# Performance work log

Measured on AMD Instinct MI355X. Metric: run time of the kernel, lower is better.

Reference implementation:

```python
import jax, jax.numpy as jnp
import numpy as np

IMG = 14          # image_x_y_dim
STRIDE = 4        # stride == kernel_size == n_qubits
H_MAT = jnp.array([[1.0, 1.0], [1.0, -1.0]], dtype=jnp.complex64) / np.sqrt(2.0)
_RZ_SIGNS = jnp.array([-0.5j, 0.5j], dtype=jnp.complex64)


def _apply_1q(state, U, w):
    # contract 2x2 gate U into wire-axis w of state with shape (2,)*n
    s = jnp.tensordot(U, state, axes=[[1], [w]])
    return jnp.moveaxis(s, 0, w)


def _rz(state, theta, w, n):
    d = jnp.exp(_RZ_SIGNS * theta)  # diag(e^{-i t/2}, e^{i t/2})
    shape = [1] * n
    shape[w] = 2
    return state * d.reshape(shape)


def _rx(state, theta, w):
    c = jnp.cos(0.5 * theta).astype(jnp.complex64)
    s = ((-1j) * jnp.sin(0.5 * theta)).astype(jnp.complex64)
    U = jnp.stack([jnp.stack([c, s]), jnp.stack([s, c])])
    return _apply_1q(state, U, w)


def _ry(state, theta, w):
    c = jnp.cos(0.5 * theta).astype(jnp.complex64)
    s = jnp.sin(0.5 * theta).astype(jnp.complex64)
    U = jnp.stack([jnp.stack([c, -s]), jnp.stack([s, c])])
    return _apply_1q(state, U, w)


def _crz(state, theta, cw, tw, n):
    # PennyLane CRZ: diag(1, 1, e^{-i t/2}, e^{i t/2}) in |control, target> basis
    d = jnp.exp(_RZ_SIGNS * theta)
    P = jnp.stack([jnp.ones(2, jnp.complex64), d])  # axes: (control, target)
    if cw > tw:
        P = P.T
    a, b = min(cw, tw), max(cw, tw)
    shape = [1] * n
    shape[a] = 2
    shape[b] = 2
    return state * P.reshape(shape)


def _zexp(state, n):
    probs = state.real ** 2 + state.imag ** 2
    outs = []
    for w in range(n):
        shape = [1] * n
        shape[w] = 2
        sgn = jnp.array([1.0, -1.0], jnp.float32).reshape(shape)
        outs.append(jnp.sum(probs * sgn))
    return jnp.stack(outs)  # (n,)


def _circuit4(x, weights):
    # x: (L,) with L in {4, 8, 16}; weights: (2, 8)
    n, vpq, L = 4, 4, x.shape[0]
    state = jnp.zeros((2,) * n, jnp.complex64).at[(0,) * n].set(1.0)
    for q in range(n):  # encoding: H then alternating RZ/RX per qubit
        state = _apply_1q(state, H_MAT, q)
        for i in range(vpq):
            idx = q * vpq + i
            if idx < L:
                state = _rz(state, x[idx], q, n) if i % 2 == 0 else _rx(state, x[idx], q)
    for l in range(2):  # n_layers
        for i in range(n):
            state = _crz(state, weights[l, i], i, (i + 1) % n, n)
        for j in range(n, 2 * n):
            state = _ry(state, weights[l, j], j % n)
    return _zexp(state, n)  # (4,)


def _circuit8(x, weights):
    # x: (64,); weights: (3, 16); angles scaled by pi as in qnn_circuit
    n, L = 8, 64
    vpq = L // n + 1  # 9
    state = jnp.zeros((2,) * n, jnp.complex64).at[(0,) * n].set(1.0)
    for q in range(n):
        state = _apply_1q(state, H_MAT, q)
        for i in range(vpq):
            idx = q * vpq + i
            if idx < L:
                theta = np.pi * x[idx]
                state = _rz(state, theta, q, n) if i % 2 == 0 else _rx(state, theta, q)
    for l in range(3):  # qnn_layers
        for i in range(n):
            state = _crz(state, weights[l, i], i, (i + 1) % n, n)
        for j in range(n, 2 * n):
            state = _ry(state, weights[l, j], j % n)
    return _zexp(state, n)  # (8,)


def _forward_single(x196, w1, w2, fc_w, fc_b):
    img = x196.reshape(IMG, IMG)
    feats = []
    for i in range(0, IMG, STRIDE):
        for j in range(0, IMG, STRIDE):
            patch = img[i:i + 4, j:j + 4].reshape(-1)  # edge patches truncate to 8 or 4
            feats.append(_circuit4(patch, w1))
    f = jnp.concatenate(feats)       # (64,)
    g = _circuit8(f, w2)             # (8,)
    return fc_w @ g + fc_b           # (3,)


def setup_inputs() -> dict:
    key = jax.random.key(0)
    k0, k1, k2, k3, k4 = jax.random.split(key, 5)
    bs = 8192
    X = jax.random.normal(k0, (bs, 196), jnp.float32)
    w1 = jax.random.uniform(k1, (2, 8), jnp.float32, 0.0, 2.0 * np.pi)
    w2 = jax.random.uniform(k2, (3, 16), jnp.float32, 0.0, 2.0 * np.pi)
    fc_w = jax.random.normal(k3, (3, 8), jnp.float32) / np.sqrt(8.0)
    fc_b = jax.random.normal(k4, (3,), jnp.float32) * 0.01
    return {"X": X, "w1": w1, "w2": w2, "fc_w": fc_w, "fc_b": fc_b}


def reference(X, w1, w2, fc_w, fc_b):
    return jax.vmap(_forward_single, in_axes=(0, None, None, None, None))(X, w1, w2, fc_w, fc_b)
```

## Files before the change

### kernel.cpp

```cpp
#include <hip/hip_runtime.h>

#define DEV __device__ __forceinline__

namespace {

typedef float f32x2 __attribute__((ext_vector_type(2)));

DEV f32x2 splat(float x){ f32x2 r; r.x = x; r.y = x; return r; }
DEV f32x2 csw(f32x2 a){ return __builtin_shufflevector(a, a, 1, 0); }
DEV f32x2 cmulv(f32x2 a, f32x2 b){
  f32x2 nt; nt.x = -b.y; nt.y = b.x;
  return splat(a.x)*b + splat(a.y)*nt;
}
DEV f32x2 cconj(f32x2 a){ a.y = -a.y; return a; }
DEV f32x2 cphase(f32x2 a, f32x2 cv, f32x2 sv){ return cv*a + sv*csw(a); }
DEV void halfsc(float th, float& c, float& s){ __sincosf(0.5f*th, &s, &c); }

constexpr float RSQRT2 = 0.70710678118654752440f;
constexpr float PI_F   = 3.14159265358979323846f;

template<int CTRL> DEV float qperm(float v){
  return __int_as_float(__builtin_amdgcn_mov_dpp(__float_as_int(v), CTRL, 0xF, 0xF, true));
}
template<int OFF> DEV float swzf(float v){
  return __int_as_float(__builtin_amdgcn_ds_swizzle(__float_as_int(v), OFF));
}
template<int B> DEV float shfx(float v){
  if constexpr (B==1)      return qperm<0xB1>(v);
  else if constexpr (B==2) return qperm<0x4E>(v);
  else if constexpr (B==4) return swzf<0x101F>(v);
  else if constexpr (B==8) return qperm<0x128>(v);
  else                     return swzf<0x401F>(v);
}

template<int I0, int N> DEV void run_gates(f32x2 (&v)[2], const float* f, float scale){
  #pragma unroll
  for (int i = I0; i < I0 + N; ++i){
    float c, s; halfsc(scale * f[i], c, s);
    f32x2 cv = splat(c);
    f32x2 sp; sp.x = s;  sp.y = -s;
    if ((i & 1) == 0){
      f32x2 sn; sn.x = -s; sn.y = s;
      v[0] = cv*v[0] + sp*csw(v[0]);
      v[1] = cv*v[1] + sn*csw(v[1]);
    } else {
      f32x2 t0 = csw(v[0]), t1 = csw(v[1]);
      v[0] = cv*v[0] + sp*t1;
      v[1] = cv*v[1] + sp*t0;
    }
  }
}
template<int N> DEV void build_psi(f32x2 (&v)[2], const float* ang, float scale){
  v[0].x = RSQRT2; v[0].y = 0.f;
  v[1].x = RSQRT2; v[1].y = 0.f;
  run_gates<0, N>(v, ang, scale);
}

template<int S> DEV void ry_loc8(f32x2 (&a)[8], float2 cs){
  const float c = cs.x, s = cs.y;
  #pragma unroll
  for (int m = 0; m < 8; ++m) if (!(m & S)) {
    f32x2 u = a[m], v = a[m|S];
    a[m]   = splat(c)*u - splat(s)*v;
    a[m|S] = splat(s)*u + splat(c)*v;
  }
}
template<int MASK> DEV void ry_lane8(f32x2 (&a)[8], int r, float2 cs){
  const float c = cs.x;
  const float sg = (r & MASK) ? cs.y : -cs.y;
  #pragma unroll
  for (int m = 0; m < 8; ++m){
    f32x2 o; o.x = shfx<MASK>(a[m].x); o.y = shfx<MASK>(a[m].y);
    a[m] = splat(c)*a[m] + splat(sg)*o;
  }
}

DEV f32x2 tov(float2 v){ f32x2 r; r.x = v.x; r.y = v.y; return r; }

}

__global__ __launch_bounds__(256, 5)
void qnn_fused_kernel(const float* __restrict__ X,  const float* __restrict__ w1,
                      const float* __restrict__ w2, const float* __restrict__ fcw,
                      const float* __restrict__ fcb, float* __restrict__ out, int bs)
{
  __shared__ float  feats[8][80];
  __shared__ float4 p1chain[8][16][5];
  __shared__ float4 chainH[8][8][2];
  __shared__ float4 chain2[8][9];
  __shared__ float4 p1phi[2][2][8];
  __shared__ float2 p1ry[2][4];
  __shared__ float2 ryw[3][8];
  __shared__ float4 phi2[3*32*9];

  const int t  = threadIdx.x;
  const int sl = t >> 5;
  const int r  = t & 31;
  int sample = blockIdx.x * 8 + sl;
  if (sample >= bs) sample = bs - 1;

  if (t < 32){
    const int l = t >> 4, Lb = (t >> 3) & 1, m = t & 7;
    const float h0 = 0.5f*w1[l*8+0], h1 = 0.5f*w1[l*8+1];
    const float h2 = 0.5f*w1[l*8+2], h3 = 0.5f*w1[l*8+3];
    const bool m4 = m & 4, m2 = m & 2, m1 = m & 1;
    float phi = 0.f;
    phi += Lb ? (m4 ? h0 : -h0) : 0.f;
    phi += m4 ? (m2 ? h1 : -h1) : 0.f;
    phi += m2 ? (m1 ? h2 : -h2) : 0.f;
    phi += m1 ? (Lb ? h3 : -h3) : 0.f;
    float c, s; __sincosf(phi, &s, &c);
    p1phi[l][Lb][m] = {c, c, -s, s};
  } else if (t < 40){
    const int j = t - 32, l = j >> 2, i = j & 3;
    float c, s; halfsc(w1[l*8 + 4 + i], c, s); p1ry[l][i] = {c, s};
  } else if (t < 64){
    const int j = t - 40, l = j >> 3, i = j & 7;
    float c, s; halfsc(w2[l*16 + 8 + i], c, s); ryw[l][i] = {c, s};
  }
  for (int idx = t; idx < 3*256; idx += 256){
    const int l = idx >> 8, rr = (idx >> 3) & 31, mm = idx & 7;
    const float* wl = w2 + l*16;
    const float h0 = 0.5f*wl[0], h1 = 0.5f*wl[1], h2 = 0.5f*wl[2], h3 = 0.5f*wl[3];
    const float h4 = 0.5f*wl[4], h5 = 0.5f*wl[5], h6 = 0.5f*wl[6], h7 = 0.5f*wl[7];
    const bool b16 = rr & 16, b8 = rr & 8, b4 = rr & 4, b2 = rr & 2, b1 = rr & 1;
    const bool m4 = mm & 4, m2 = mm & 2, m1 = mm & 1;
    float phi = 0.f;
    phi += b16 ? (b8 ? h0 : -h0) : 0.f;
    phi += b8  ? (b4 ? h1 : -h1) : 0.f;
    phi += b4  ? (b2 ? h2 : -h2) : 0.f;
    phi += b2  ? (b1 ? h3 : -h3) : 0.f;
    phi += b1  ? (m4 ? h4 : -h4) : 0.f;
    phi += m4  ? (m2 ? h5 : -h5) : 0.f;
    phi += m2  ? (m1 ? h6 : -h6) : 0.f;
    phi += m1  ? (b16 ? h7 : -h7) : 0.f;
    float c, s; __sincosf(phi, &s, &c);
    phi2[(l*32 + rr)*9 + mm] = {c, c, -s, s};
  }

  #pragma unroll
  for (int jj = 0; jj < 2; ++jj){
    const int j = t + jj*256;
    const int s_ = j >> 6, p = (j >> 2) & 15, q = j & 3;
    const int pi = p >> 2, pj = p & 3;
    const int shift = (pj == 3) ? 1 : 2;
    const int cmask = (1 << shift) - 1;
    const int limit = ((pi == 3) ? 2 : 4) << shift;
    int gs = blockIdx.x * 8 + s_;
    if (gs >= bs) gs = bs - 1;
    const float* Xf = X + (size_t)gs * 196;
    float ang[4];
    #pragma unroll
    for (int i = 0; i < 4; ++i){
      const int k = q*4 + i;
      int idx = (pi*4 + (k >> shift))*14 + pj*4 + (k & cmask);
      idx = idx > 195 ? 195 : idx;
      float v = Xf[idx];
      ang[i] = (k < limit) ? v : 0.f;
    }
    f32x2 v[2];
    build_psi<4>(v, ang, 1.0f);
    p1chain[s_][p][q] = {v[0].x, v[0].y, v[1].x, v[1].y};
  }
  __syncthreads();

  {
    const int p = r >> 1, Lb = r & 1;
    f32x2 ps[4][2];
    #pragma unroll
    for (int q = 0; q < 4; ++q){
      float4 fq = p1chain[sl][p][q];
      ps[q][0].x = fq.x; ps[q][0].y = fq.y;
      ps[q][1].x = fq.z; ps[q][1].y = fq.w;
    }
    f32x2 a8[8];
    {
      f32x2 t12[4];
      #pragma unroll
      for (int j = 0; j < 4; ++j) t12[j] = cmulv(ps[1][j>>1], ps[2][j&1]);
      f32x2 base = Lb ? ps[0][1] : ps[0][0];
      f32x2 bt[4];
      #pragma unroll
      for (int j = 0; j < 4; ++j) bt[j] = cmulv(base, t12[j]);
      #pragma unroll
      for (int m = 0; m < 8; ++m) a8[m] = cmulv(bt[m>>1], ps[3][m&1]);
    }

    #pragma unroll
    for (int l = 0; l < 2; ++l){
      const float4* ph = &p1phi[l][Lb][0];
      #pragma unroll
      for (int m = 0; m < 8; ++m){
        float4 w = ph[m];
        f32x2 cv; cv.x = w.x; cv.y = w.y;
        f32x2 sv; sv.x = w.z; sv.y = w.w;
        a8[m] = cphase(a8[m], cv, sv);
      }
      ry_lane8<1>(a8, r, p1ry[l][0]);
      ry_loc8<4>(a8, p1ry[l][1]);
      ry_loc8<2>(a8, p1ry[l][2]);
      ry_loc8<1>(a8, p1ry[l][3]);
    }

    float pr8[8];
    #pragma unroll
    for (int m = 0; m < 8; ++m) pr8[m] = a8[m].x*a8[m].x + a8[m].y*a8[m].y;
    float s_loc = 0.f;
    #pragma unroll
    for (int m = 0; m < 8; ++m) s_loc += pr8[m];
    float e1 = 0.f, e2 = 0.f, e3 = 0.f;
    #pragma unroll
    for (int m = 0; m < 8; ++m){
      e1 += (m & 4) ? -pr8[m] : pr8[m];
      e2 += (m & 2) ? -pr8[m] : pr8[m];
      e3 += (m & 1) ? -pr8[m] : pr8[m];
    }
    float v0 = Lb ? -s_loc : s_loc;
    v0 += shfx<1>(v0); e1 += shfx<1>(e1); e2 += shfx<1>(e2); e3 += shfx<1>(e3);
    feats[sl][p*4 + 2*Lb + 0] = Lb ? e2 : v0;
    feats[sl][p*4 + 2*Lb + 1] = Lb ? e3 : e1;
    if (r < 16) feats[sl][64 + r] = 0.f;
  }
  __syncthreads();

  if (t < 128){
    const int h = t >> 6, jj = t & 63;
    const int s_ = jj >> 3, c = jj & 7;
    const float* f = &feats[s_][c*9];
    f32x2 v[2];
    if (h == 0){
      build_psi<5>(v, f, PI_F);
    } else {
      v[0].x = 1.f; v[0].y = 0.f;
      v[1].x = 0.f; v[1].y = 0.f;
      run_gates<5, 4>(v, f, PI_F);
    }
    chainH[s_][c][h] = {v[0].x, v[0].y, v[1].x, v[1].y};
  }
  __syncthreads();
  if (t < 64){
    const int s_ = t >> 3, c = t & 7;
    float4 A = chainH[s_][c][0], B = chainH[s_][c][1];
    f32x2 vA0, vA1, al, be;
    vA0.x=A.x; vA0.y=A.y; vA1.x=A.z; vA1.y=A.w;
    al.x=B.x;  al.y=B.y;  be.x=B.z;  be.y=B.w;
    f32x2 v0 = cmulv(al, vA0) - cmulv(cconj(be), vA1);
    f32x2 v1 = cmulv(be, vA0) + cmulv(cconj(al), vA1);
    chain2[s_][c] = {v0.x, v0.y, v1.x, v1.y};
  }
  __syncthreads();

  f32x2 a[8];
  {
    const float2* c2 = (const float2*)&chain2[sl][0];
    f32x2 e0 = tov(c2[0*2 + ((r>>4)&1)]);
    f32x2 e1 = tov(c2[1*2 + ((r>>3)&1)]);
    f32x2 e2 = tov(c2[2*2 + ((r>>2)&1)]);
    f32x2 e3 = tov(c2[3*2 + ((r>>1)&1)]);
    f32x2 e4 = tov(c2[4*2 + ( r    &1)]);
    f32x2 L  = cmulv(cmulv(cmulv(e0, e1), cmulv(e2, e3)), e4);

    float4 q5 = chain2[sl][5], q6 = chain2[sl][6], q7 = chain2[sl][7];
    f32x2 p5[2], p6[2], p7[2];
    p5[0].x=q5.x; p5[0].y=q5.y; p5[1].x=q5.z; p5[1].y=q5.w;
    p6[0].x=q6.x; p6[0].y=q6.y; p6[1].x=q6.z; p6[1].y=q6.w;
    p7[0].x=q7.x; p7[0].y=q7.y; p7[1].x=q7.z; p7[1].y=q7.w;
    f32x2 p56[4];
    #pragma unroll
    for (int j = 0; j < 4; ++j) p56[j] = cmulv(p5[j>>1], p6[j&1]);
    f32x2 Lp[4];
    #pragma unroll
    for (int j = 0; j < 4; ++j) Lp[j] = cmulv(L, p56[j]);
    #pragma unroll
    for (int m = 0; m < 8; ++m) a[m] = cmulv(Lp[m>>1], p7[m&1]);
  }

  #pragma unroll
  for (int l = 0; l < 3; ++l){
    const float4* ph = &phi2[(l*32 + r)*9];
    #pragma unroll
    for (int m = 0; m < 8; ++m){
      float4 w = ph[m];
      f32x2 cv; cv.x = w.x; cv.y = w.y;
      f32x2 sv; sv.x = w.z; sv.y = w.w;
      a[m] = cphase(a[m], cv, sv);
    }
    ry_lane8<16>(a, r, ryw[l][0]);
    ry_lane8<8>(a, r, ryw[l][1]);
    ry_lane8<4>(a, r, ryw[l][2]);
    ry_lane8<2>(a, r, ryw[l][3]);
    ry_lane8<1>(a, r, ryw[l][4]);
    ry_loc8<4>(a, ryw[l][5]);
    ry_loc8<2>(a, ryw[l][6]);
    ry_loc8<1>(a, ryw[l][7]);
  }

  float pr8[8];
  #pragma unroll
  for (int m = 0; m < 8; ++m) pr8[m] = a[m].x*a[m].x + a[m].y*a[m].y;
  float s_loc = 0.f;
  #pragma unroll
  for (int m = 0; m < 8; ++m) s_loc += pr8[m];
  float e5 = 0.f, e6 = 0.f, e7 = 0.f;
  #pragma unroll
  for (int m = 0; m < 8; ++m){
    e5 += (m & 4) ? -pr8[m] : pr8[m];
    e6 += (m & 2) ? -pr8[m] : pr8[m];
    e7 += (m & 1) ? -pr8[m] : pr8[m];
  }
  float gp[8];
  gp[0] = (r & 16) ? -s_loc : s_loc;
  gp[1] = (r &  8) ? -s_loc : s_loc;
  gp[2] = (r &  4) ? -s_loc : s_loc;
  gp[3] = (r &  2) ? -s_loc : s_loc;
  gp[4] = (r &  1) ? -s_loc : s_loc;
  gp[5] = e5; gp[6] = e6; gp[7] = e7;

  float o0 = 0.f, o1 = 0.f, o2 = 0.f;
  #pragma unroll
  for (int w = 0; w < 8; ++w){
    o0 += fcw[0*8 + w] * gp[w];
    o1 += fcw[1*8 + w] * gp[w];
    o2 += fcw[2*8 + w] * gp[w];
  }
  o0 += shfx<1>(o0);  o1 += shfx<1>(o1);  o2 += shfx<1>(o2);
  o0 += shfx<2>(o0);  o1 += shfx<2>(o1);  o2 += shfx<2>(o2);
  o0 += shfx<4>(o0);  o1 += shfx<4>(o1);  o2 += shfx<4>(o2);
  o0 += shfx<8>(o0);  o1 += shfx<8>(o1);  o2 += shfx<8>(o2);
  o0 += shfx<16>(o0); o1 += shfx<16>(o1); o2 += shfx<16>(o2);

  if (r < 3){
    float o = (r == 0) ? o0 : ((r == 1) ? o1 : o2);
    out[(size_t)sample*3 + r] = o + fcb[r];
  }
}

extern "C" void kernel_launch(void* const* d_in, const int* in_sizes, int n_in,
                              void* d_out, int out_size, void* d_ws, size_t ws_size,
                              hipStream_t stream)
{
  const float* X   = (const float*)d_in[0];
  const float* w1  = (const float*)d_in[1];
  const float* w2  = (const float*)d_in[2];
  const float* fcw = (const float*)d_in[3];
  const float* fcb = (const float*)d_in[4];
  float* out = (float*)d_out;
  const int bs = in_sizes[0] / 196;
  const int blocks = (bs + 7) / 8;
  hipLaunchKernelGGL(qnn_fused_kernel, dim3(blocks), dim3(256), 0, stream,
                     X, w1, w2, fcw, fcb, out, bs);
}
```

Measured before the change: 17.99 us.

## Process 16 samples per block with 16 amplitudes per lane

```diff
diff --git a/kernel.cpp b/kernel.cpp
--- a/kernel.cpp
+++ b/kernel.cpp
@@ -13,7 +13,10 @@
   return splat(a.x)*b + splat(a.y)*nt;
 }
 DEV f32x2 cconj(f32x2 a){ a.y = -a.y; return a; }
-DEV f32x2 cphase(f32x2 a, f32x2 cv, f32x2 sv){ return cv*a + sv*csw(a); }
+DEV f32x2 cphase2(f32x2 a, float c, float s){
+  f32x2 sv; sv.x = -s; sv.y = s;
+  return splat(c)*a + sv*csw(a);
+}
 DEV void halfsc(float th, float& c, float& s){ __sincosf(0.5f*th, &s, &c); }
 
 constexpr float RSQRT2 = 0.70710678118654752440f;
@@ -29,8 +32,7 @@
   if constexpr (B==1)      return qperm<0xB1>(v);
   else if constexpr (B==2) return qperm<0x4E>(v);
   else if constexpr (B==4) return swzf<0x101F>(v);
-  else if constexpr (B==8) return qperm<0x128>(v);
-  else                     return swzf<0x401F>(v);
+  else                     return qperm<0x128>(v);
 }
 
 template<int I0, int N> DEV void run_gates(f32x2 (&v)[2], const float* f, float scale){
@@ -56,20 +58,20 @@
   run_gates<0, N>(v, ang, scale);
 }
 
-template<int S> DEV void ry_loc8(f32x2 (&a)[8], float2 cs){
+template<int S> DEV void ry_loc16(f32x2 (&a)[16], float2 cs){
   const float c = cs.x, s = cs.y;
   #pragma unroll
-  for (int m = 0; m < 8; ++m) if (!(m & S)) {
+  for (int m = 0; m < 16; ++m) if (!(m & S)) {
     f32x2 u = a[m], v = a[m|S];
     a[m]   = splat(c)*u - splat(s)*v;
     a[m|S] = splat(s)*u + splat(c)*v;
   }
 }
-template<int MASK> DEV void ry_lane8(f32x2 (&a)[8], int r, float2 cs){
+template<int MASK> DEV void ry_lane16(f32x2 (&a)[16], int r, float2 cs){
   const float c = cs.x;
   const float sg = (r & MASK) ? cs.y : -cs.y;
   #pragma unroll
-  for (int m = 0; m < 8; ++m){
+  for (int m = 0; m < 16; ++m){
     f32x2 o; o.x = shfx<MASK>(a[m].x); o.y = shfx<MASK>(a[m].y);
     a[m] = splat(c)*a[m] + splat(sg)*o;
   }
@@ -79,38 +81,38 @@
 
 }
 
-__global__ __launch_bounds__(256, 5)
+__global__ __launch_bounds__(256, 2)
 void qnn_fused_kernel(const float* __restrict__ X,  const float* __restrict__ w1,
                       const float* __restrict__ w2, const float* __restrict__ fcw,
                       const float* __restrict__ fcb, float* __restrict__ out, int bs)
 {
-  __shared__ float  feats[8][80];
-  __shared__ float4 p1chain[8][16][5];
-  __shared__ float4 chainH[8][8][2];
-  __shared__ float4 chain2[8][9];
-  __shared__ float4 p1phi[2][2][8];
+  __shared__ float  feats[16][80];
+  __shared__ float4 p1chain[16][16][5];
+  __shared__ float4 chainH[16][8][2];
+  __shared__ float4 chain2[16][9];
+  __shared__ float2 p1phi2[2][16];
   __shared__ float2 p1ry[2][4];
   __shared__ float2 ryw[3][8];
-  __shared__ float4 phi2[3*32*9];
+  __shared__ float2 phi2[3*16*18];
 
   const int t  = threadIdx.x;
-  const int sl = t >> 5;
-  const int r  = t & 31;
-  int sample = blockIdx.x * 8 + sl;
+  const int sl = t >> 4;
+  const int r  = t & 15;
+  int sample = blockIdx.x * 16 + sl;
   if (sample >= bs) sample = bs - 1;
 
   if (t < 32){
-    const int l = t >> 4, Lb = (t >> 3) & 1, m = t & 7;
+    const int l = t >> 4, m = t & 15;
     const float h0 = 0.5f*w1[l*8+0], h1 = 0.5f*w1[l*8+1];
     const float h2 = 0.5f*w1[l*8+2], h3 = 0.5f*w1[l*8+3];
-    const bool m4 = m & 4, m2 = m & 2, m1 = m & 1;
+    const bool b0 = m & 8, b1 = m & 4, b2 = m & 2, b3 = m & 1;
     float phi = 0.f;
-    phi += Lb ? (m4 ? h0 : -h0) : 0.f;
-    phi += m4 ? (m2 ? h1 : -h1) : 0.f;
-    phi += m2 ? (m1 ? h2 : -h2) : 0.f;
-    phi += m1 ? (Lb ? h3 : -h3) : 0.f;
+    phi += b0 ? (b1 ? h0 : -h0) : 0.f;
+    phi += b1 ? (b2 ? h1 : -h1) : 0.f;
+    phi += b2 ? (b3 ? h2 : -h2) : 0.f;
+    phi += b3 ? (b0 ? h3 : -h3) : 0.f;
     float c, s; __sincosf(phi, &s, &c);
-    p1phi[l][Lb][m] = {c, c, -s, s};
+    p1phi2[l][m] = {c, s};
   } else if (t < 40){
     const int j = t - 32, l = j >> 2, i = j & 3;
     float c, s; halfsc(w1[l*8 + 4 + i], c, s); p1ry[l][i] = {c, s};
@@ -118,35 +120,34 @@
     const int j = t - 40, l = j >> 3, i = j & 7;
     float c, s; halfsc(w2[l*16 + 8 + i], c, s); ryw[l][i] = {c, s};
   }
-  for (int idx = t; idx < 3*256; idx += 256){
-    const int l = idx >> 8, rr = (idx >> 3) & 31, mm = idx & 7;
+  #pragma unroll
+  for (int jj = 0; jj < 3; ++jj){
+    const int idx = t + jj*256;
+    const int l = idx >> 8, rr = (idx >> 4) & 15, mm = idx & 15;
     const float* wl = w2 + l*16;
-    const float h0 = 0.5f*wl[0], h1 = 0.5f*wl[1], h2 = 0.5f*wl[2], h3 = 0.5f*wl[3];
-    const float h4 = 0.5f*wl[4], h5 = 0.5f*wl[5], h6 = 0.5f*wl[6], h7 = 0.5f*wl[7];
-    const bool b16 = rr & 16, b8 = rr & 8, b4 = rr & 4, b2 = rr & 2, b1 = rr & 1;
-    const bool m4 = mm & 4, m2 = mm & 2, m1 = mm & 1;
+    float h[8];
+    #pragma unroll
+    for (int i = 0; i < 8; ++i) h[i] = 0.5f*wl[i];
+    bool b[8];
+    b[0]=(rr>>3)&1; b[1]=(rr>>2)&1; b[2]=(rr>>1)&1; b[3]=rr&1;
+    b[4]=(mm>>3)&1; b[5]=(mm>>2)&1; b[6]=(mm>>1)&1; b[7]=mm&1;
     float phi = 0.f;
-    phi += b16 ? (b8 ? h0 : -h0) : 0.f;
-    phi += b8  ? (b4 ? h1 : -h1) : 0.f;
-    phi += b4  ? (b2 ? h2 : -h2) : 0.f;
-    phi += b2  ? (b1 ? h3 : -h3) : 0.f;
-    phi += b1  ? (m4 ? h4 : -h4) : 0.f;
-    phi += m4  ? (m2 ? h5 : -h5) : 0.f;
-    phi += m2  ? (m1 ? h6 : -h6) : 0.f;
-    phi += m1  ? (b16 ? h7 : -h7) : 0.f;
+    #pragma unroll
+    for (int i = 0; i < 8; ++i)
+      phi += b[i] ? (b[(i+1)&7] ? h[i] : -h[i]) : 0.f;
     float c, s; __sincosf(phi, &s, &c);
-    phi2[(l*32 + rr)*9 + mm] = {c, c, -s, s};
-  }
-
-  #pragma unroll
-  for (int jj = 0; jj < 2; ++jj){
+    phi2[(l*16 + rr)*18 + mm] = {c, s};
+  }
+
+  #pragma unroll
+  for (int jj = 0; jj < 4; ++jj){
     const int j = t + jj*256;
     const int s_ = j >> 6, p = (j >> 2) & 15, q = j & 3;
     const int pi = p >> 2, pj = p & 3;
     const int shift = (pj == 3) ? 1 : 2;
     const int cmask = (1 << shift) - 1;
     const int limit = ((pi == 3) ? 2 : 4) << shift;
-    int gs = blockIdx.x * 8 + s_;
+    int gs = blockIdx.x * 16 + s_;
     if (gs >= bs) gs = bs - 1;
     const float* Xf = X + (size_t)gs * 196;
     float ang[4];
@@ -165,67 +166,56 @@
   __syncthreads();
 
   {
-    const int p = r >> 1, Lb = r & 1;
     f32x2 ps[4][2];
     #pragma unroll
     for (int q = 0; q < 4; ++q){
-      float4 fq = p1chain[sl][p][q];
+      float4 fq = p1chain[sl][r][q];
       ps[q][0].x = fq.x; ps[q][0].y = fq.y;
       ps[q][1].x = fq.z; ps[q][1].y = fq.w;
     }
-    f32x2 a8[8];
+    f32x2 a[16];
     {
-      f32x2 t12[4];
+      f32x2 T01[4], T23[4];
       #pragma unroll
-      for (int j = 0; j < 4; ++j) t12[j] = cmulv(ps[1][j>>1], ps[2][j&1]);
-      f32x2 base = Lb ? ps[0][1] : ps[0][0];
-      f32x2 bt[4];
+      for (int j = 0; j < 4; ++j){
+        T01[j] = cmulv(ps[0][j>>1], ps[1][j&1]);
+        T23[j] = cmulv(ps[2][j>>1], ps[3][j&1]);
+      }
       #pragma unroll
-      for (int j = 0; j < 4; ++j) bt[j] = cmulv(base, t12[j]);
+      for (int m = 0; m < 16; ++m) a[m] = cmulv(T01[m>>2], T23[m&3]);
+    }
+
+    #pragma unroll
+    for (int l = 0; l < 2; ++l){
+      const float4* ph4 = (const float4*)&p1phi2[l][0];
       #pragma unroll
-      for (int m = 0; m < 8; ++m) a8[m] = cmulv(bt[m>>1], ps[3][m&1]);
-    }
-
-    #pragma unroll
-    for (int l = 0; l < 2; ++l){
-      const float4* ph = &p1phi[l][Lb][0];
+      for (int j = 0; j < 8; ++j){
+        float4 w = ph4[j];
+        a[2*j]   = cphase2(a[2*j],   w.x, w.y);
+        a[2*j+1] = cphase2(a[2*j+1], w.z, w.w);
+      }
+      ry_loc16<8>(a, p1ry[l][0]); ry_loc16<4>(a, p1ry[l][1]);
+      ry_loc16<2>(a, p1ry[l][2]); ry_loc16<1>(a, p1ry[l][3]);
+    }
+
+    float pr[16];
+    #pragma unroll
+    for (int m = 0; m < 16; ++m) pr[m] = a[m].x*a[m].x + a[m].y*a[m].y;
+    #pragma unroll
+    for (int w = 0; w < 4; ++w){
+      const int S = 8 >> w;
+      float e = 0.f;
       #pragma unroll
-      for (int m = 0; m < 8; ++m){
-        float4 w = ph[m];
-        f32x2 cv; cv.x = w.x; cv.y = w.y;
-        f32x2 sv; sv.x = w.z; sv.y = w.w;
-        a8[m] = cphase(a8[m], cv, sv);
-      }
-      ry_lane8<1>(a8, r, p1ry[l][0]);
-      ry_loc8<4>(a8, p1ry[l][1]);
-      ry_loc8<2>(a8, p1ry[l][2]);
-      ry_loc8<1>(a8, p1ry[l][3]);
-    }
-
-    float pr8[8];
-    #pragma unroll
-    for (int m = 0; m < 8; ++m) pr8[m] = a8[m].x*a8[m].x + a8[m].y*a8[m].y;
-    float s_loc = 0.f;
-    #pragma unroll
-    for (int m = 0; m < 8; ++m) s_loc += pr8[m];
-    float e1 = 0.f, e2 = 0.f, e3 = 0.f;
-    #pragma unroll
-    for (int m = 0; m < 8; ++m){
-      e1 += (m & 4) ? -pr8[m] : pr8[m];
-      e2 += (m & 2) ? -pr8[m] : pr8[m];
-      e3 += (m & 1) ? -pr8[m] : pr8[m];
-    }
-    float v0 = Lb ? -s_loc : s_loc;
-    v0 += shfx<1>(v0); e1 += shfx<1>(e1); e2 += shfx<1>(e2); e3 += shfx<1>(e3);
-    feats[sl][p*4 + 2*Lb + 0] = Lb ? e2 : v0;
-    feats[sl][p*4 + 2*Lb + 1] = Lb ? e3 : e1;
-    if (r < 16) feats[sl][64 + r] = 0.f;
+      for (int m = 0; m < 16; ++m) e += (m & S) ? -pr[m] : pr[m];
+      feats[sl][r*4 + w] = e;
+    }
+    feats[sl][64 + r] = 0.f;
   }
   __syncthreads();
 
-  if (t < 128){
-    const int h = t >> 6, jj = t & 63;
-    const int s_ = jj >> 3, c = jj & 7;
+  {
+    const int h = t >> 7, idx = t & 127;
+    const int s_ = idx >> 3, c = idx & 7;
     const float* f = &feats[s_][c*9];
     f32x2 v[2];
     if (h == 0){
@@ -238,7 +228,7 @@
     chainH[s_][c][h] = {v[0].x, v[0].y, v[1].x, v[1].y};
   }
   __syncthreads();
-  if (t < 64){
+  if (t < 128){
     const int s_ = t >> 3, c = t & 7;
     float4 A = chainH[s_][c][0], B = chainH[s_][c][1];
     f32x2 vA0, vA1, al, be;
@@ -250,71 +240,73 @@
   }
   __syncthreads();
 
-  f32x2 a[8];
+  f32x2 a[16];
   {
     const float2* c2 = (const float2*)&chain2[sl][0];
-    f32x2 e0 = tov(c2[0*2 + ((r>>4)&1)]);
-    f32x2 e1 = tov(c2[1*2 + ((r>>3)&1)]);
-    f32x2 e2 = tov(c2[2*2 + ((r>>2)&1)]);
-    f32x2 e3 = tov(c2[3*2 + ((r>>1)&1)]);
-    f32x2 e4 = tov(c2[4*2 + ( r    &1)]);
-    f32x2 L  = cmulv(cmulv(cmulv(e0, e1), cmulv(e2, e3)), e4);
-
-    float4 q5 = chain2[sl][5], q6 = chain2[sl][6], q7 = chain2[sl][7];
-    f32x2 p5[2], p6[2], p7[2];
+    f32x2 e0 = tov(c2[0*2 + ((r>>3)&1)]);
+    f32x2 e1 = tov(c2[1*2 + ((r>>2)&1)]);
+    f32x2 e2 = tov(c2[2*2 + ((r>>1)&1)]);
+    f32x2 e3 = tov(c2[3*2 + ( r    &1)]);
+    f32x2 L  = cmulv(cmulv(e0, e1), cmulv(e2, e3));
+
+    float4 q4 = chain2[sl][4], q5 = chain2[sl][5];
+    float4 q6 = chain2[sl][6], q7 = chain2[sl][7];
+    f32x2 p4[2], p5[2], p6[2], p7[2];
+    p4[0].x=q4.x; p4[0].y=q4.y; p4[1].x=q4.z; p4[1].y=q4.w;
     p5[0].x=q5.x; p5[0].y=q5.y; p5[1].x=q5.z; p5[1].y=q5.w;
     p6[0].x=q6.x; p6[0].y=q6.y; p6[1].x=q6.z; p6[1].y=q6.w;
     p7[0].x=q7.x; p7[0].y=q7.y; p7[1].x=q7.z; p7[1].y=q7.w;
-    f32x2 p56[4];
-    #pragma unroll
-    for (int j = 0; j < 4; ++j) p56[j] = cmulv(p5[j>>1], p6[j&1]);
+    f32x2 p45[4], p67[4];
+    #pragma unroll
+    for (int j = 0; j < 4; ++j){
+      p45[j] = cmulv(p4[j>>1], p5[j&1]);
+      p67[j] = cmulv(p6[j>>1], p7[j&1]);
+    }
     f32x2 Lp[4];
     #pragma unroll
-    for (int j = 0; j < 4; ++j) Lp[j] = cmulv(L, p56[j]);
-    #pragma unroll
-    for (int m = 0; m < 8; ++m) a[m] = cmulv(Lp[m>>1], p7[m&1]);
+    for (int j = 0; j < 4; ++j) Lp[j] = cmulv(L, p45[j]);
+    #pragma unroll
+    for (int m = 0; m < 16; ++m) a[m] = cmulv(Lp[m>>2], p67[m&3]);
   }
 
   #pragma unroll
   for (int l = 0; l < 3; ++l){
-    const float4* ph = &phi2[(l*32 + r)*9];
-    #pragma unroll
-    for (int m = 0; m < 8; ++m){
-      float4 w = ph[m];
-      f32x2 cv; cv.x = w.x; cv.y = w.y;
-      f32x2 sv; sv.x = w.z; sv.y = w.w;
-      a[m] = cphase(a[m], cv, sv);
-    }
-    ry_lane8<16>(a, r, ryw[l][0]);
-    ry_lane8<8>(a, r, ryw[l][1]);
-    ry_lane8<4>(a, r, ryw[l][2]);
-    ry_lane8<2>(a, r, ryw[l][3]);
-    ry_lane8<1>(a, r, ryw[l][4]);
-    ry_loc8<4>(a, ryw[l][5]);
-    ry_loc8<2>(a, ryw[l][6]);
-    ry_loc8<1>(a, ryw[l][7]);
-  }
-
-  float pr8[8];
-  #pragma unroll
-  for (int m = 0; m < 8; ++m) pr8[m] = a[m].x*a[m].x + a[m].y*a[m].y;
-  float s_loc = 0.f;
-  #pragma unroll
-  for (int m = 0; m < 8; ++m) s_loc += pr8[m];
-  float e5 = 0.f, e6 = 0.f, e7 = 0.f;
-  #pragma unroll
-  for (int m = 0; m < 8; ++m){
-    e5 += (m & 4) ? -pr8[m] : pr8[m];
-    e6 += (m & 2) ? -pr8[m] : pr8[m];
-    e7 += (m & 1) ? -pr8[m] : pr8[m];
-  }
+    const float4* ph4 = (const float4*)&phi2[(l*16 + r)*18];
+    #pragma unroll
+    for (int j = 0; j < 8; ++j){
+      float4 w = ph4[j];
+      a[2*j]   = cphase2(a[2*j],   w.x, w.y);
+      a[2*j+1] = cphase2(a[2*j+1], w.z, w.w);
+    }
+    ry_lane16<8>(a, r, ryw[l][0]);
+    ry_lane16<4>(a, r, ryw[l][1]);
+    ry_lane16<2>(a, r, ryw[l][2]);
+    ry_lane16<1>(a, r, ryw[l][3]);
+    ry_loc16<8>(a, ryw[l][4]);
+    ry_loc16<4>(a, ryw[l][5]);
+    ry_loc16<2>(a, ryw[l][6]);
+    ry_loc16<1>(a, ryw[l][7]);
+  }
+
+  float pr[16];
+  #pragma unroll
+  for (int m = 0; m < 16; ++m) pr[m] = a[m].x*a[m].x + a[m].y*a[m].y;
+  float Ssum = 0.f;
+  #pragma unroll
+  for (int m = 0; m < 16; ++m) Ssum += pr[m];
   float gp[8];
-  gp[0] = (r & 16) ? -s_loc : s_loc;
-  gp[1] = (r &  8) ? -s_loc : s_loc;
-  gp[2] = (r &  4) ? -s_loc : s_loc;
-  gp[3] = (r &  2) ? -s_loc : s_loc;
-  gp[4] = (r &  1) ? -s_loc : s_loc;
-  gp[5] = e5; gp[6] = e6; gp[7] = e7;
+  gp[0] = (r & 8) ? -Ssum : Ssum;
+  gp[1] = (r & 4) ? -Ssum : Ssum;
+  gp[2] = (r & 2) ? -Ssum : Ssum;
+  gp[3] = (r & 1) ? -Ssum : Ssum;
+  #pragma unroll
+  for (int w = 4; w < 8; ++w){
+    const int S = 8 >> (w-4);
+    float e = 0.f;
+    #pragma unroll
+    for (int m = 0; m < 16; ++m) e += (m & S) ? -pr[m] : pr[m];
+    gp[w] = e;
+  }
 
   float o0 = 0.f, o1 = 0.f, o2 = 0.f;
   #pragma unroll
@@ -323,11 +315,10 @@
     o1 += fcw[1*8 + w] * gp[w];
     o2 += fcw[2*8 + w] * gp[w];
   }
-  o0 += shfx<1>(o0);  o1 += shfx<1>(o1);  o2 += shfx<1>(o2);
-  o0 += shfx<2>(o0);  o1 += shfx<2>(o1);  o2 += shfx<2>(o2);
-  o0 += shfx<4>(o0);  o1 += shfx<4>(o1);  o2 += shfx<4>(o2);
-  o0 += shfx<8>(o0);  o1 += shfx<8>(o1);  o2 += shfx<8>(o2);
-  o0 += shfx<16>(o0); o1 += shfx<16>(o1); o2 += shfx<16>(o2);
+  o0 += shfx<1>(o0); o1 += shfx<1>(o1); o2 += shfx<1>(o2);
+  o0 += shfx<2>(o0); o1 += shfx<2>(o1); o2 += shfx<2>(o2);
+  o0 += shfx<4>(o0); o1 += shfx<4>(o1); o2 += shfx<4>(o2);
+  o0 += shfx<8>(o0); o1 += shfx<8>(o1); o2 += shfx<8>(o2);
 
   if (r < 3){
     float o = (r == 0) ? o0 : ((r == 1) ? o1 : o2);
@@ -346,7 +337,7 @@
   const float* fcb = (const float*)d_in[4];
   float* out = (float*)d_out;
   const int bs = in_sizes[0] / 196;
-  const int blocks = (bs + 7) / 8;
+  const int blocks = (bs + 15) / 16;
   hipLaunchKernelGGL(qnn_fused_kernel, dim3(blocks), dim3(256), 0, stream,
                      X, w1, w2, fcw, fcb, out, bs);
 }
```

Result: faster. 17.05 us (-5.2%).
